# Kernel optimization log

Hardware: AMD Instinct MI355X
Metric: run time of the kernel (lower is better)

The kernel has to match this reference:

```python
import jax, jax.numpy as jnp
import numpy as np

DIM = 192
NUM_HEADS = 6
WH, WW = 7, 7
N = WH * WW  # 49 tokens per window
C2 = 2 * DIM  # concatenated channel dim = 384
SCALE = (DIM // NUM_HEADS) ** -0.5  # module uses dim//num_heads, not C2//num_heads
NW = 64  # number of windows per image
B_ = 2048  # num_windows * batch


def _relative_position_index():
    ch = np.arange(WH)
    cw = np.arange(WW)
    coords = np.stack(np.meshgrid(ch, cw, indexing='ij')).reshape(2, -1)  # [2, N]
    rel = coords[:, :, None] - coords[:, None, :]  # [2, N, N]
    rel = rel.transpose(1, 2, 0).astype(np.int64)  # [N, N, 2]
    rel[..., 0] += WH - 1
    rel[..., 1] += WW - 1
    rel[..., 0] *= 2 * WW - 1
    return jnp.asarray(rel.sum(-1))  # [N, N]

REL_IDX = _relative_position_index()


def setup_inputs() -> dict:
    key = jax.random.key(0)
    ks = jax.random.split(key, 8)
    x = jax.random.normal(ks[0], (B_, N, DIM), dtype=jnp.float32)
    y = jax.random.normal(ks[1], (B_, N, DIM), dtype=jnp.float32)
    mask = jax.random.normal(ks[2], (NW, N, N), dtype=jnp.float32)
    w_qkv = jax.random.normal(ks[3], (6 * DIM, C2), dtype=jnp.float32) * 0.02
    b_qkv = jnp.zeros((6 * DIM,), dtype=jnp.float32)
    w_proj = jax.random.normal(ks[4], (DIM, C2), dtype=jnp.float32) * 0.02
    b_proj = jnp.zeros((DIM,), dtype=jnp.float32)
    bias_table = jax.random.normal(ks[5], ((2 * WH - 1) * (2 * WW - 1), NUM_HEADS), dtype=jnp.float32) * 0.02
    return {"x": x, "y": y, "mask": mask, "w_qkv": w_qkv, "b_qkv": b_qkv,
            "w_proj": w_proj, "b_proj": b_proj, "bias_table": bias_table}


def reference(x, y, mask, w_qkv, b_qkv, w_proj, b_proj, bias_table):
    Bc = x.shape[0]
    Dh = C2 // NUM_HEADS  # 64
    xy = jnp.concatenate([x, y], axis=2)  # [B_, N, 2*dim]
    qkv = xy @ w_qkv.T + b_qkv  # [B_, N, 6*dim]
    qkv = qkv.reshape(Bc, N, 3, NUM_HEADS, Dh).transpose(2, 0, 3, 1, 4)  # [3, B_, H, N, Dh]
    q, k, v = qkv[0] * SCALE, qkv[1], qkv[2]
    attn = jnp.einsum('bhnd,bhmd->bhnm', q, k)  # [B_, H, N, N]
    rpb = bias_table[REL_IDX]  # [N, N, H]
    attn = attn + rpb.transpose(2, 0, 1)[None]
    nW = mask.shape[0]
    attn = attn.reshape(Bc // nW, nW, NUM_HEADS, N, N) + mask[None, :, None]
    attn = attn.reshape(Bc, NUM_HEADS, N, N)
    attn = jax.nn.softmax(attn, axis=-1)
    out = jnp.einsum('bhnm,bhmd->bhnd', attn, v)  # [B_, H, N, Dh]
    out = out.transpose(0, 2, 1, 3).reshape(Bc, N, C2)
    return out @ w_proj.T + b_proj  # [B_, N, dim]
```

## Files before the change

### kernel.cpp

```cpp
#include <hip/hip_runtime.h>
#include <hip/hip_bf16.h>


typedef __attribute__((ext_vector_type(8))) short short8;
typedef __attribute__((ext_vector_type(4))) float f32x4;

#define SCALE 0.17677669529663687f

#define WQF_OFF    0ul
#define WQF_BYTES  (864ul*1024)
#define WPF_OFF    (WQF_OFF + WQF_BYTES)
#define WPF_BYTES  (144ul*1024)
#define COMB_OFF   (WPF_OFF + WPF_BYTES)
#define COMB_BYTES (64ul*6*4096*4)
#define WS_NEED    (COMB_OFF + COMB_BYTES)

__device__ __forceinline__ unsigned short f2bf(float f){
  unsigned u = __builtin_bit_cast(unsigned, f);
  u = u + 0x7fffu + ((u >> 16) & 1u);
  return (unsigned short)(u >> 16);
}
__device__ __forceinline__ unsigned long long pack4(float4 v){
  return (unsigned long long)f2bf(v.x) | ((unsigned long long)f2bf(v.y) << 16)
       | ((unsigned long long)f2bf(v.z) << 32) | ((unsigned long long)f2bf(v.w) << 48);
}

__device__ __forceinline__ unsigned short cvt1(float x){
  unsigned r;
  asm("v_cvt_pk_bf16_f32 %0, %1, %1" : "=v"(r) : "v"(x));
  return (unsigned short)r;
}
__device__ __forceinline__ uint2 pk4(float a, float b, float c, float d){
  unsigned lo, hi;
  asm("v_cvt_pk_bf16_f32 %0, %1, %2" : "=v"(lo) : "v"(a), "v"(b));
  asm("v_cvt_pk_bf16_f32 %0, %1, %2" : "=v"(hi) : "v"(c), "v"(d));
  return make_uint2(lo, hi);
}

__global__ void k0_wfrag(const float* __restrict__ wq_f, const float* __restrict__ wp_f,
                         unsigned short* __restrict__ wqf, unsigned short* __restrict__ wpf){
  int t = blockIdx.x*256 + threadIdx.x;
  int fragidx = t >> 6, l = t & 63;
  const float* src; unsigned short* dst;
  float sc = 1.0f;
  if (fragidx < 864){
    int h = fragidx/144, rem = fragidx - h*144;
    int ct = rem/12, kt = rem - ct*12;
    int row = (ct>>2)*384 + h*64 + (ct&3)*16 + (l&15);
    src = wq_f + (long)row*384 + kt*32 + (l>>4)*8;
    dst = wqf + (long)fragidx*512 + l*8;
    if (ct < 4) sc = SCALE;
  } else {
    int fid = fragidx - 864;
    int ct = fid/12, kt = fid - ct*12;
    int row = ct*16 + (l&15);
    src = wp_f + (long)row*384 + kt*32 + (l>>4)*8;
    dst = wpf + (long)fid*512 + l*8;
  }
  short8 v;
  #pragma unroll
  for (int e = 0; e < 8; ++e) v[e] = (short)f2bf(src[e] * sc);
  *(short8*)dst = v;
}

__global__ void prep_comb(const float* __restrict__ mask, const float* __restrict__ btab,
                          float* __restrict__ comb){
  int idx = blockIdx.x * 256 + threadIdx.x;
  int j = idx & 63, i = (idx >> 6) & 63, rest = idx >> 12;
  int h = rest % 6, w = rest / 6;
  float v;
  if (i < 49 && j < 49){
    int di = i / 7 - j / 7 + 6;
    int dj = i % 7 - j % 7 + 6;
    v = btab[(di * 13 + dj) * 6 + h] + mask[(w * 49 + i) * 49 + j];
  } else {
    v = (j >= 49) ? -1e30f : 0.0f;
  }
  comb[idx] = v;
}

__device__ __forceinline__ int swz(int r, int b){ return b ^ ((r & 7) << 4); }
__device__ __forceinline__ int a_q (int r, int c){ return 49152 + swz(r, r*128 + c*2); }
__device__ __forceinline__ int a_k (int r, int c){ return 57344 + swz(r, r*128 + c*2); }
__device__ __forceinline__ int a_vt(int r, int c){ return 65536 + swz(r, r*128 + c*2); }
#define OBUF 73728

__global__ __launch_bounds__(256, 2)
void k_fused(const float* __restrict__ x, const float* __restrict__ y,
             const unsigned short* __restrict__ wqf, const unsigned short* __restrict__ wpf,
             const float* __restrict__ bqkv, const float* __restrict__ bproj,
             const float* __restrict__ comb, float* __restrict__ out){
  __shared__ __align__(16) unsigned char smem[81920];
  const int win = blockIdx.x;
  const int tid = threadIdx.x, w = tid>>6, l = tid&63, l15 = l&15, lg = l>>4;

  for (int t = tid; t < 2352; t += 256){
    int r = t / 48, c8 = t - r*48;
    int c = c8*8;
    const float* src = (c < 192) ? (x + ((long)win*49 + r)*192 + c)
                                 : (y + ((long)win*49 + r)*192 + (c - 192));
    float4 f0 = *(const float4*)src, f1 = *(const float4*)(src + 4);
    uint2 lo = pk4(f0.x, f0.y, f0.z, f0.w);
    uint2 hi = pk4(f1.x, f1.y, f1.z, f1.w);
    uint4 vv = make_uint4(lo.x, lo.y, hi.x, hi.y);
    int addr = (c8>>2)*4096 + (r>>4)*1024 + (((r&15) + (c8&3)*16))*16;
    *(uint4*)(smem + addr) = vv;
  }
  for (int t = tid; t < 720; t += 256){
    int rr = t / 48, c8 = t - rr*48;
    int r = 49 + rr;
    int addr = (c8>>2)*4096 + (r>>4)*1024 + (((r&15) + (c8&3)*16))*16;
    *(uint4*)(smem + addr) = make_uint4(0,0,0,0);
  }

  int np[3];
  f32x4 pacc[4][3];
  #pragma unroll
  for (int nt = 0; nt < 3; ++nt){
    np[nt] = w*48 + nt*16 + l15;
    float bv = bproj[np[nt]];
    #pragma unroll
    for (int mt = 0; mt < 4; ++mt)
      #pragma unroll
      for (int j = 0; j < 4; ++j) pacc[mt][nt][j] = (mt == 0 && j == 0) ? bv : ((mt==0&&j==0)?bv:0.0f);
  }
  #pragma unroll
  for (int nt = 0; nt < 3; ++nt){
    float bv = bproj[np[nt]];
    #pragma unroll
    for (int mt = 0; mt < 4; ++mt)
      #pragma unroll
      for (int j = 0; j < 4; ++j) pacc[mt][nt][j] = bv;
  }

  __syncthreads();

  #pragma unroll 1
  for (int h = 0; h < 6; ++h){
    const float* cb = comb + ((long)((win & 63)*6 + h))*4096 + (w*16 + l15)*64 + lg*4;
    float4 cbv[4];
    #pragma unroll
    for (int nt = 0; nt < 4; ++nt) cbv[nt] = *(const float4*)(cb + nt*16);

    float bias[3];
    #pragma unroll
    for (int nt = 0; nt < 3; ++nt){
      int ct = w*3 + nt, s = ct >> 2;
      bias[nt] = bqkv[s*384 + h*64 + (ct & 3)*16 + l15];
      if (s == 0) bias[nt] *= SCALE;
    }

    const unsigned short* Bb = wqf + ((long)h*12 + w*3)*12*512;
    short8 bB[2][3];
    #pragma unroll
    for (int nt = 0; nt < 3; ++nt) bB[0][nt] = *(const short8*)(Bb + (nt*12)*512 + l*8);
    f32x4 acc[4][3];
    #pragma unroll
    for (int mt = 0; mt < 4; ++mt)
      #pragma unroll
      for (int nt = 0; nt < 3; ++nt)
        #pragma unroll
        for (int j = 0; j < 4; ++j) acc[mt][nt][j] = bias[nt];

    #pragma unroll
    for (int kt = 0; kt < 12; ++kt){
      const int cur = kt & 1, nxt = cur ^ 1;
      if (kt < 11){
        #pragma unroll
        for (int nt = 0; nt < 3; ++nt)
          bB[nxt][nt] = *(const short8*)(Bb + (nt*12 + kt+1)*512 + l*8);
      }
      short8 aA[4];
      #pragma unroll
      for (int mt = 0; mt < 4; ++mt)
        aA[mt] = *(const short8*)(smem + (kt*4 + mt)*1024 + l*16);
      __builtin_amdgcn_sched_barrier(0);
      __builtin_amdgcn_s_setprio(1);
      #pragma unroll
      for (int nt = 0; nt < 3; ++nt){
        #pragma unroll
        for (int mt = 0; mt < 4; ++mt)
          acc[mt][nt] = __builtin_amdgcn_mfma_f32_16x16x32_bf16(aA[mt], bB[cur][nt], acc[mt][nt], 0, 0, 0);
      }
      __builtin_amdgcn_s_setprio(0);
    }

    #pragma unroll
    for (int nt = 0; nt < 3; ++nt){
      int ct = w*3 + nt, s = ct >> 2, d16 = (ct & 3) * 16;
      if (s == 2){
        #pragma unroll
        for (int mt = 0; mt < 4; ++mt){
          uint2 p = pk4(acc[mt][nt][0], acc[mt][nt][1], acc[mt][nt][2], acc[mt][nt][3]);
          *(uint2*)(smem + a_vt(d16 + l15, mt*16 + lg*4)) = p;
        }
      } else {
        #pragma unroll
        for (int mt = 0; mt < 4; ++mt){
          #pragma unroll
          for (int j = 0; j < 4; ++j){
            int row = mt*16 + lg*4 + j;
            int addr = (s == 0) ? a_q(row, d16 + l15) : a_k(row, d16 + l15);
            *(unsigned short*)(smem + addr) = cvt1(acc[mt][nt][j]);
          }
        }
      }
    }
    __syncthreads();

    short8 bq[2];
    #pragma unroll
    for (int ks = 0; ks < 2; ++ks)
      bq[ks] = *(const short8*)(smem + a_q(w*16 + l15, ks*32 + lg*8));
    f32x4 st[4] = {};
    __builtin_amdgcn_s_setprio(1);
    #pragma unroll
    for (int ks = 0; ks < 2; ++ks){
      #pragma unroll
      for (int nt = 0; nt < 4; ++nt){
        short8 ak = *(const short8*)(smem + a_k(nt*16 + l15, ks*32 + lg*8));
        st[nt] = __builtin_amdgcn_mfma_f32_16x16x32_bf16(ak, bq[ks], st[nt], 0, 0, 0);
      }
    }
    __builtin_amdgcn_s_setprio(0);
    #pragma unroll
    for (int nt = 0; nt < 4; ++nt){
      st[nt][0] += cbv[nt].x; st[nt][1] += cbv[nt].y;
      st[nt][2] += cbv[nt].z; st[nt][3] += cbv[nt].w;
    }
    float mx;
    {
      float m0 = fmaxf(fmaxf(st[0][0], st[0][1]), fmaxf(st[0][2], st[0][3]));
      float m1 = fmaxf(fmaxf(st[1][0], st[1][1]), fmaxf(st[1][2], st[1][3]));
      float m2 = fmaxf(fmaxf(st[2][0], st[2][1]), fmaxf(st[2][2], st[2][3]));
      float m3 = fmaxf(fmaxf(st[3][0], st[3][1]), fmaxf(st[3][2], st[3][3]));
      mx = fmaxf(fmaxf(m0, m1), fmaxf(m2, m3));
    }
    mx = fmaxf(mx, __shfl_xor(mx, 16));
    mx = fmaxf(mx, __shfl_xor(mx, 32));
    float ssum = 0.f;
    #pragma unroll
    for (int nt = 0; nt < 4; ++nt){
      #pragma unroll
      for (int j = 0; j < 4; ++j){
        float e = __expf(st[nt][j] - mx);
        st[nt][j] = e; ssum += e;
      }
    }
    ssum += __shfl_xor(ssum, 16);
    ssum += __shfl_xor(ssum, 32);
    const float inv = 1.0f / ssum;

    #pragma unroll
    for (int nt = 0; nt < 4; ++nt){
      uint2 p = pk4(st[nt][0]*inv, st[nt][1]*inv, st[nt][2]*inv, st[nt][3]*inv);
      *(uint2*)(smem + a_q(w*16 + l15, nt*16 + lg*4)) = p;
    }

    short8 ap[2];
    #pragma unroll
    for (int ks = 0; ks < 2; ++ks)
      ap[ks] = *(const short8*)(smem + a_q(w*16 + l15, ks*32 + lg*8));
    f32x4 oacc[4] = {};
    __builtin_amdgcn_s_setprio(1);
    #pragma unroll
    for (int ks = 0; ks < 2; ++ks){
      #pragma unroll
      for (int nt = 0; nt < 4; ++nt){
        short8 bv = *(const short8*)(smem + a_vt(nt*16 + l15, ks*32 + lg*8));
        oacc[nt] = __builtin_amdgcn_mfma_f32_16x16x32_bf16(ap[ks], bv, oacc[nt], 0, 0, 0);
      }
    }
    __builtin_amdgcn_s_setprio(0);
    #pragma unroll
    for (int nt = 0; nt < 4; ++nt){
      int frag  = (nt >> 1)*4 + w;
      int chunk0 = (lg*4) + ((nt & 1)*2 + (l15 >> 3))*16;
      #pragma unroll
      for (int j = 0; j < 4; ++j){
        int addr = OBUF + frag*1024 + (chunk0 + j)*16 + (l15 & 7)*2;
        *(unsigned short*)(smem + addr) = cvt1(oacc[nt][j]);
      }
    }
    __syncthreads();

    #pragma unroll
    for (int ks = 0; ks < 2; ++ks){
      short8 aO[4];
      #pragma unroll
      for (int mt = 0; mt < 4; ++mt)
        aO[mt] = *(const short8*)(smem + OBUF + (ks*4 + mt)*1024 + l*16);
      __builtin_amdgcn_s_setprio(1);
      #pragma unroll
      for (int nt = 0; nt < 3; ++nt){
        short8 bb = *(const short8*)(wpf + ((long)(w*3 + nt)*12 + h*2 + ks)*512 + l*8);
        #pragma unroll
        for (int mt = 0; mt < 4; ++mt)
          pacc[mt][nt] = __builtin_amdgcn_mfma_f32_16x16x32_bf16(aO[mt], bb, pacc[mt][nt], 0, 0, 0);
      }
      __builtin_amdgcn_s_setprio(0);
    }
  }

  #pragma unroll
  for (int mt = 0; mt < 4; ++mt){
    #pragma unroll
    for (int j = 0; j < 4; ++j){
      int row = mt*16 + lg*4 + j;
      if (row < 49){
        float* o = out + ((long)win*49 + row)*192;
        #pragma unroll
        for (int nt = 0; nt < 3; ++nt)
          o[np[nt]] = pacc[mt][nt][j];
      }
    }
  }
}

#define FB_WQ_ELEMS (1152*384)
#define FB_WP_ELEMS (192*384)
#define FB_WP_OFF   (FB_WQ_ELEMS*2)
#define FB_COMB_OFF (FB_WP_OFF + FB_WP_ELEMS*2)

__global__ void prep_weights_fb(const float* __restrict__ wq_f, const float* __restrict__ wp_f,
                                unsigned short* __restrict__ wq, unsigned short* __restrict__ wp){
  int gid = blockIdx.x * 256 + threadIdx.x;
  if (gid < FB_WQ_ELEMS) wq[gid] = f2bf(wq_f[gid]);
  else { int g = gid - FB_WQ_ELEMS; if (g < FB_WP_ELEMS) wp[g] = f2bf(wp_f[g]); }
}
__device__ __forceinline__ int fb_xy(int r, int c){ return 0      + swz(r, r*768 + c*2); }
__device__ __forceinline__ int fb_q (int r, int c){ return 49152  + swz(r, r*128 + c*2); }
__device__ __forceinline__ int fb_k (int r, int c){ return 57344  + swz(r, r*128 + c*2); }
__device__ __forceinline__ int fb_vt(int r, int c){ return 65536  + swz(r, r*128 + c*2); }
__device__ __forceinline__ int fb_p (int r, int c){ return 73728  + swz(r, r*128 + c*2); }

__global__ __launch_bounds__(256, 2)
void fused_attn_fb(const float* __restrict__ x, const float* __restrict__ y,
                   const float* __restrict__ bqkv, const float* __restrict__ bproj,
                   const unsigned short* __restrict__ wq, const unsigned short* __restrict__ wp,
                   const float* __restrict__ comb, float* __restrict__ out){
  __shared__ __align__(16) unsigned char smem[81920];
  const int b = blockIdx.x, tid = threadIdx.x;
  const int w = tid>>6, l = tid&63, l15 = l&15, lg = l>>4;
  {
    const float4* x4 = (const float4*)x + b * 2352;
    const float4* y4 = (const float4*)y + b * 2352;
    for (int idx = tid; idx < 2352; idx += 256){
      int r = idx / 48, c4 = (idx % 48) * 4;
      float4 vx = x4[idx], vy = y4[idx];
      *(unsigned long long*)(smem + fb_xy(r, c4))       = pack4(vx);
      *(unsigned long long*)(smem + fb_xy(r, 192 + c4)) = pack4(vy);
    }
    for (int idx = tid; idx < 1440; idx += 256){
      int r = 49 + idx / 96, c4 = (idx % 96) * 4;
      *(unsigned long long*)(smem + fb_xy(r, c4)) = 0ull;
    }
  }
  __syncthreads();
  const float* cbB = comb + (long)(b & 63) * (6 * 4096);
  f32x4 pacc[4][3] = {};
  int np[3]; float bp[3];
  #pragma unroll
  for (int nt = 0; nt < 3; ++nt){ np[nt] = w*48 + nt*16 + l15; bp[nt] = bproj[np[nt]]; }
  #pragma unroll 1
  for (int h = 0; h < 6; ++h){
    f32x4 acc[4][3] = {};
    int wrow[3]; float bias[3];
    #pragma unroll
    for (int nt = 0; nt < 3; ++nt){
      int n = np[nt];
      wrow[nt] = (n >> 6) * 384 + h * 64 + (n & 63);
      bias[nt] = bqkv[wrow[nt]];
    }
    #pragma unroll 4
    for (int kt = 0; kt < 12; ++kt){
      int k0 = kt * 32;
      short8 a[4];
      #pragma unroll
      for (int mt = 0; mt < 4; ++mt)
        a[mt] = *(const short8*)(smem + fb_xy(mt*16 + l15, k0 + lg*8));
      #pragma unroll
      for (int nt = 0; nt < 3; ++nt){
        short8 bb = *(const short8*)(wq + (long)wrow[nt]*384 + k0 + lg*8);
        #pragma unroll
        for (int mt = 0; mt < 4; ++mt)
          acc[mt][nt] = __builtin_amdgcn_mfma_f32_16x16x32_bf16(a[mt], bb, acc[mt][nt], 0, 0, 0);
      }
    }
    #pragma unroll
    for (int nt = 0; nt < 3; ++nt){
      int n = np[nt], s = n >> 6, d = n & 63;
      #pragma unroll
      for (int mt = 0; mt < 4; ++mt){
        #pragma unroll
        for (int j = 0; j < 4; ++j){
          int row = mt*16 + lg*4 + j;
          float v = acc[mt][nt][j] + bias[nt];
          if (s == 0) v *= SCALE;
          int addr = (s==0) ? fb_q(row,d) : (s==1) ? fb_k(row,d) : fb_vt(d,row);
          *(unsigned short*)(smem + addr) = f2bf(v);
        }
      }
    }
    __syncthreads();
    short8 aq[2];
    #pragma unroll
    for (int ks = 0; ks < 2; ++ks)
      aq[ks] = *(const short8*)(smem + fb_q(w*16 + l15, ks*32 + lg*8));
    f32x4 sacc[4] = {};
    #pragma unroll
    for (int ks = 0; ks < 2; ++ks)
      #pragma unroll
      for (int nt = 0; nt < 4; ++nt){
        short8 bk = *(const short8*)(smem + fb_k(nt*16 + l15, ks*32 + lg*8));
        sacc[nt] = __builtin_amdgcn_mfma_f32_16x16x32_bf16(aq[ks], bk, sacc[nt], 0, 0, 0);
      }
    const float* cb = cbB + h * 4096;
    float rs[4];
    #pragma unroll
    for (int j = 0; j < 4; ++j){
      int r = w*16 + lg*4 + j;
      #pragma unroll
      for (int nt = 0; nt < 4; ++nt) sacc[nt][j] += cb[r*64 + nt*16 + l15];
      float m = fmaxf(fmaxf(sacc[0][j], sacc[1][j]), fmaxf(sacc[2][j], sacc[3][j]));
      #pragma unroll
      for (int dlt = 1; dlt < 16; dlt <<= 1) m = fmaxf(m, __shfl_xor(m, dlt));
      float ssum = 0.f;
      #pragma unroll
      for (int nt = 0; nt < 4; ++nt){
        float e = __expf(sacc[nt][j] - m);
        sacc[nt][j] = e; ssum += e;
      }
      #pragma unroll
      for (int dlt = 1; dlt < 16; dlt <<= 1) ssum += __shfl_xor(ssum, dlt);
      rs[j] = ssum;
      #pragma unroll
      for (int nt = 0; nt < 4; ++nt)
        *(unsigned short*)(smem + fb_p(r, nt*16 + l15)) = f2bf(sacc[nt][j]);
    }
    short8 ap[2];
    #pragma unroll
    for (int ks = 0; ks < 2; ++ks)
      ap[ks] = *(const short8*)(smem + fb_p(w*16 + l15, ks*32 + lg*8));
    f32x4 oacc[4] = {};
    #pragma unroll
    for (int ks = 0; ks < 2; ++ks)
      #pragma unroll
      for (int nt = 0; nt < 4; ++nt){
        short8 bv = *(const short8*)(smem + fb_vt(nt*16 + l15, ks*32 + lg*8));
        oacc[nt] = __builtin_amdgcn_mfma_f32_16x16x32_bf16(ap[ks], bv, oacc[nt], 0, 0, 0);
      }
    float inv[4];
    #pragma unroll
    for (int j = 0; j < 4; ++j) inv[j] = 1.0f / rs[j];
    #pragma unroll
    for (int nt = 0; nt < 4; ++nt)
      #pragma unroll
      for (int j = 0; j < 4; ++j){
        int row = w*16 + lg*4 + j;
        *(unsigned short*)(smem + fb_p(row, nt*16 + l15)) = f2bf(oacc[nt][j] * inv[j]);
      }
    __syncthreads();
    #pragma unroll
    for (int ks = 0; ks < 2; ++ks){
      short8 ao8[4];
      #pragma unroll
      for (int mt = 0; mt < 4; ++mt)
        ao8[mt] = *(const short8*)(smem + fb_p(mt*16 + l15, ks*32 + lg*8));
      #pragma unroll
      for (int nt = 0; nt < 3; ++nt){
        short8 bb = *(const short8*)(wp + (long)np[nt]*384 + h*64 + ks*32 + lg*8);
        #pragma unroll
        for (int mt = 0; mt < 4; ++mt)
          pacc[mt][nt] = __builtin_amdgcn_mfma_f32_16x16x32_bf16(ao8[mt], bb, pacc[mt][nt], 0, 0, 0);
      }
    }
  }
  #pragma unroll
  for (int mt = 0; mt < 4; ++mt)
    #pragma unroll
    for (int j = 0; j < 4; ++j){
      int row = mt*16 + lg*4 + j;
      if (row < 49){
        float* o = out + ((long)b*49 + row)*192;
        #pragma unroll
        for (int nt = 0; nt < 3; ++nt)
          o[np[nt]] = pacc[mt][nt][j] + bp[nt];
      }
    }
}

extern "C" void kernel_launch(void* const* d_in, const int* in_sizes, int n_in,
                              void* d_out, int out_size, void* d_ws, size_t ws_size,
                              hipStream_t stream){
  (void)in_sizes; (void)n_in; (void)out_size;
  const float* x     = (const float*)d_in[0];
  const float* y     = (const float*)d_in[1];
  const float* mask  = (const float*)d_in[2];
  const float* wq_f  = (const float*)d_in[3];
  const float* bqkv  = (const float*)d_in[4];
  const float* wp_f  = (const float*)d_in[5];
  const float* bproj = (const float*)d_in[6];
  const float* btab  = (const float*)d_in[7];
  float* out = (float*)d_out;

  if (ws_size >= WS_NEED){
    unsigned short* wqf = (unsigned short*)((char*)d_ws + WQF_OFF);
    unsigned short* wpf = (unsigned short*)((char*)d_ws + WPF_OFF);
    float*          cmb = (float*)((char*)d_ws + COMB_OFF);
    hipLaunchKernelGGL(k0_wfrag,  dim3(252),  dim3(256), 0, stream, wq_f, wp_f, wqf, wpf);
    hipLaunchKernelGGL(prep_comb, dim3(6144), dim3(256), 0, stream, mask, btab, cmb);
    hipLaunchKernelGGL(k_fused,   dim3(2048), dim3(256), 0, stream,
                       x, y, wqf, wpf, bqkv, bproj, cmb, out);
  } else {
    unsigned short* wq  = (unsigned short*)d_ws;
    unsigned short* wp  = (unsigned short*)((char*)d_ws + FB_WP_OFF);
    float*          cmb = (float*)((char*)d_ws + FB_COMB_OFF);
    hipLaunchKernelGGL(prep_weights_fb, dim3(2016), dim3(256), 0, stream, wq_f, wp_f, wq, wp);
    hipLaunchKernelGGL(prep_comb,       dim3(6144), dim3(256), 0, stream, mask, btab, cmb);
    hipLaunchKernelGGL(fused_attn_fb,   dim3(2048), dim3(256), 0, stream,
                       x, y, bqkv, bproj, wq, wp, cmb, out);
  }
}
```

Measured before the change: 220.9 us.

## Remap activation staging to fragment order and double-buffer LDS A-fragment loads

The x/y staging loop is reorganised so each wave fills whole 1KB fragment tiles with a fixed unrolled 12-iteration loop, folding the zero padding of rows 49..63 into the same pass instead of a separate loop with integer divisions. In the QKV GEMM, A fragments from LDS are now prefetched one k-step ahead into a double buffer, matching the existing B-fragment prefetch, so LDS latency overlaps the MFMAs. A dead duplicate bias-initialisation loop is removed. The extra buffer raises register pressure under launch_bounds(256,2).

Result: slower. 256.1 us (+15.9%).

```diff
diff --git a/kernel.cpp b/kernel.cpp
--- a/kernel.cpp
+++ b/kernel.cpp
@@ -94,23 +94,22 @@
   const int win = blockIdx.x;
   const int tid = threadIdx.x, w = tid>>6, l = tid&63, l15 = l&15, lg = l>>4;
 
-  for (int t = tid; t < 2352; t += 256){
-    int r = t / 48, c8 = t - r*48;
-    int c = c8*8;
-    const float* src = (c < 192) ? (x + ((long)win*49 + r)*192 + c)
-                                 : (y + ((long)win*49 + r)*192 + (c - 192));
-    float4 f0 = *(const float4*)src, f1 = *(const float4*)(src + 4);
-    uint2 lo = pk4(f0.x, f0.y, f0.z, f0.w);
-    uint2 hi = pk4(f1.x, f1.y, f1.z, f1.w);
-    uint4 vv = make_uint4(lo.x, lo.y, hi.x, hi.y);
-    int addr = (c8>>2)*4096 + (r>>4)*1024 + (((r&15) + (c8&3)*16))*16;
-    *(uint4*)(smem + addr) = vv;
-  }
-  for (int t = tid; t < 720; t += 256){
-    int rr = t / 48, c8 = t - rr*48;
-    int r = 49 + rr;
-    int addr = (c8>>2)*4096 + (r>>4)*1024 + (((r&15) + (c8&3)*16))*16;
-    *(uint4*)(smem + addr) = make_uint4(0,0,0,0);
+  #pragma unroll
+  for (int i = 0; i < 12; ++i){
+    int f  = w*12 + i;
+    int kt = f >> 2, mt = f & 3;
+    int row = mt*16 + l15;
+    int c   = kt*32 + lg*8;
+    uint4 vv = make_uint4(0,0,0,0);
+    if (row < 49){
+      const float* src = (c < 192) ? (x + ((long)win*49 + row)*192 + c)
+                                   : (y + ((long)win*49 + row)*192 + (c - 192));
+      float4 f0 = *(const float4*)src, f1 = *(const float4*)(src + 4);
+      uint2 lo = pk4(f0.x, f0.y, f0.z, f0.w);
+      uint2 hi = pk4(f1.x, f1.y, f1.z, f1.w);
+      vv = make_uint4(lo.x, lo.y, hi.x, hi.y);
+    }
+    *(uint4*)(smem + f*1024 + l*16) = vv;
   }
 
   int np[3];
@@ -122,14 +121,6 @@
     #pragma unroll
     for (int mt = 0; mt < 4; ++mt)
       #pragma unroll
-      for (int j = 0; j < 4; ++j) pacc[mt][nt][j] = (mt == 0 && j == 0) ? bv : ((mt==0&&j==0)?bv:0.0f);
-  }
-  #pragma unroll
-  for (int nt = 0; nt < 3; ++nt){
-    float bv = bproj[np[nt]];
-    #pragma unroll
-    for (int mt = 0; mt < 4; ++mt)
-      #pragma unroll
       for (int j = 0; j < 4; ++j) pacc[mt][nt][j] = bv;
   }
 
@@ -151,9 +142,13 @@
     }
 
     const unsigned short* Bb = wqf + ((long)h*12 + w*3)*12*512;
-    short8 bB[2][3];
-    #pragma unroll
-    for (int nt = 0; nt < 3; ++nt) bB[0][nt] = *(const short8*)(Bb + (nt*12)*512 + l*8);
+    short8 aA[2][4], bB[2][3];
+    #pragma unroll
+    for (int mt = 0; mt < 4; ++mt)
+      aA[0][mt] = *(const short8*)(smem + mt*1024 + l*16);
+    #pragma unroll
+    for (int nt = 0; nt < 3; ++nt)
+      bB[0][nt] = *(const short8*)(Bb + (nt*12)*512 + l*8);
     f32x4 acc[4][3];
     #pragma unroll
     for (int mt = 0; mt < 4; ++mt)
@@ -169,18 +164,17 @@
         #pragma unroll
         for (int nt = 0; nt < 3; ++nt)
           bB[nxt][nt] = *(const short8*)(Bb + (nt*12 + kt+1)*512 + l*8);
-      }
-      short8 aA[4];
-      #pragma unroll
-      for (int mt = 0; mt < 4; ++mt)
-        aA[mt] = *(const short8*)(smem + (kt*4 + mt)*1024 + l*16);
+        #pragma unroll
+        for (int mt = 0; mt < 4; ++mt)
+          aA[nxt][mt] = *(const short8*)(smem + ((kt+1)*4 + mt)*1024 + l*16);
+      }
       __builtin_amdgcn_sched_barrier(0);
       __builtin_amdgcn_s_setprio(1);
       #pragma unroll
       for (int nt = 0; nt < 3; ++nt){
         #pragma unroll
         for (int mt = 0; mt < 4; ++mt)
-          acc[mt][nt] = __builtin_amdgcn_mfma_f32_16x16x32_bf16(aA[mt], bB[cur][nt], acc[mt][nt], 0, 0, 0);
+          acc[mt][nt] = __builtin_amdgcn_mfma_f32_16x16x32_bf16(aA[cur][mt], bB[cur][nt], acc[mt][nt], 0, 0, 0);
       }
       __builtin_amdgcn_s_setprio(0);
     }
```
